# Kernel optimization log

Hardware: AMD Instinct MI355X
Metric: run time of the kernel (lower is better)

Reference implementation:

```python
import jax, jax.numpy as jnp
import numpy as np

N = 100000
E = 1600000
IN_C = 128
HID = 64
HEADS = 2
OUT_C = 64
Z = 16
NEG_SLOPE = 0.2


def _gat_layer(x, src, dst, W, a_src, a_dst, b, heads, d):
    # x: [N, in], W: [in, heads*d]
    h = (x @ W).reshape(-1, heads, d)                      # [N, H, d]
    alpha_s = (h * a_src).sum(-1)                          # [N, H]
    alpha_d = (h * a_dst).sum(-1)                          # [N, H]
    e = jax.nn.leaky_relu(alpha_s[src] + alpha_d[dst], NEG_SLOPE)  # [E, H]
    m = jax.ops.segment_max(e, dst, num_segments=N)        # [N, H]
    ex = jnp.exp(e - m[dst])
    denom = jax.ops.segment_sum(ex, dst, num_segments=N)   # [N, H]
    alpha = ex / (denom[dst] + 1e-16)                      # [E, H]
    out = jax.ops.segment_sum(h[src] * alpha[:, :, None], dst, num_segments=N)  # [N, H, d]
    return out.reshape(-1, heads * d) + b


def setup_inputs() -> dict:
    key = jax.random.key(0)
    ks = jax.random.split(key, 24)
    g = lambda k, shp, fan: jax.random.normal(k, shp, jnp.float32) * (1.0 / np.sqrt(fan))
    inp = {
        "x": jax.random.normal(ks[0], (N, IN_C), jnp.float32),
        "edge_index": jax.random.randint(ks[1], (2, E), 0, N, jnp.int64),
        "edge_attr": jax.random.normal(ks[2], (E, 8), jnp.float32),
        "eps": jax.random.normal(ks[3], (N, Z), jnp.float32),
        # GAT layer 1: heads=2, d=HID
        "W1": g(ks[4], (IN_C, HEADS * HID), IN_C),
        "a_src1": g(ks[5], (HEADS, HID), HID),
        "a_dst1": g(ks[6], (HEADS, HID), HID),
        "b1": jnp.zeros((HEADS * HID,), jnp.float32),
        # GAT layer 2: heads=1, d=OUT_C
        "W2": g(ks[7], (HEADS * HID, OUT_C), HEADS * HID),
        "a_src2": g(ks[8], (1, OUT_C), OUT_C),
        "a_dst2": g(ks[9], (1, OUT_C), OUT_C),
        "b2": jnp.zeros((OUT_C,), jnp.float32),
        # VAE
        "fc1_w": g(ks[10], (64, 128), 64), "fc1_b": jnp.zeros((128,), jnp.float32),
        "mu_w": g(ks[11], (128, Z), 128), "mu_b": jnp.zeros((Z,), jnp.float32),
        "lv_w": g(ks[12], (128, Z), 128), "lv_b": jnp.zeros((Z,), jnp.float32),
        "fc3_w": g(ks[13], (Z, 128), Z), "fc3_b": jnp.zeros((128,), jnp.float32),
        "fc4_w": g(ks[14], (128, 64), 128), "fc4_b": jnp.zeros((64,), jnp.float32),
    }
    return inp


def reference(x, edge_index, edge_attr, eps, W1, a_src1, a_dst1, b1, W2, a_src2, a_dst2, b2,
              fc1_w, fc1_b, mu_w, mu_b, lv_w, lv_b, fc3_w, fc3_b, fc4_w, fc4_b):
    src, dst = edge_index[0], edge_index[1]
    # GAT stack (edge_attr ignored: GATConv edge_dim=None)
    h = jax.nn.relu(_gat_layer(x, src, dst, W1, a_src1, a_dst1, b1, HEADS, HID))
    gat_out = _gat_layer(h, src, dst, W2, a_src2, a_dst2, b2, 1, OUT_C)  # [N, 64]
    # VAE
    h1 = jax.nn.relu(gat_out @ fc1_w + fc1_b)
    mu = h1 @ mu_w + mu_b
    logvar = h1 @ lv_w + lv_b
    lv = jnp.clip(logvar, -10.0, 10.0)
    z = mu + eps * jnp.exp(0.5 * lv)
    h3 = jax.nn.relu(z @ fc3_w + fc3_b)
    recon = h3 @ fc4_w + fc4_b
    return recon, mu, logvar, gat_out
```

## Files before the change

kernel.cpp:

```cpp
#include <hip/hip_runtime.h>
#include <hip/hip_bf16.h>

typedef __attribute__((ext_vector_type(8))) short bf16x8;
typedef __attribute__((ext_vector_type(4))) float f32x4;

__device__ __forceinline__ unsigned short f2b_bits(float x) {
    __hip_bfloat16 h = __float2bfloat16(x);
    unsigned short u;
    __builtin_memcpy(&u, &h, 2);
    return u;
}
__device__ __forceinline__ unsigned int pack2(float a, float b) {
    return (unsigned int)f2b_bits(a) | ((unsigned int)f2b_bits(b) << 16);
}
__device__ __forceinline__ float sx8(unsigned int w, int b) {
    return (float)((int)(w << (24 - 8 * b)) >> 24);
}

template<int FIN, int FOUT, int EPI, int HD, bool ABF, int ACT>
__global__ __launch_bounds__(256) void mfma_k(const void* __restrict__ Av,
                                              const float* __restrict__ W,
                                              const float* __restrict__ W2,
                                              const float* __restrict__ bias,
                                              const float* __restrict__ bias2,
                                              void* __restrict__ outv,
                                              void* __restrict__ out2,
                                              void* __restrict__ out3,
                                              float* __restrict__ scales,
                                              const float* __restrict__ asr,
                                              const float* __restrict__ adr,
                                              float* __restrict__ aso,
                                              float* __restrict__ ado,
                                              const float* __restrict__ epsp,
                                              int n)
{
    constexpr int KE = (FIN < 32) ? 32 : FIN;
    constexpr int KP = KE + 8;
    constexpr int KS = KE / 32;
    constexpr int NT = FOUT / 16;
    __shared__ __align__(16) unsigned short As[64 * KP];
    __shared__ __align__(16) unsigned short Wt[FOUT * KP];

    const int t  = threadIdx.x;
    const int m0 = blockIdx.x * 64;

    for (int idx = t; idx < 64 * (KE / 4); idx += 256) {
        int r  = idx / (KE / 4);
        int c4 = (idx % (KE / 4)) * 4;
        int row = m0 + r;
        unsigned int p0 = 0, p1 = 0;
        if (row < n && c4 < FIN) {
            if constexpr (ABF) {
                uint2 rv = *(const uint2*)((const unsigned short*)Av + (size_t)row * FIN + c4);
                p0 = rv.x; p1 = rv.y;
            } else {
                float4 v = *(const float4*)((const float*)Av + (size_t)row * FIN + c4);
                p0 = pack2(v.x, v.y); p1 = pack2(v.z, v.w);
            }
        }
        *(uint2*)(As + r * KP + c4) = make_uint2(p0, p1);
    }
    for (int idx = t; idx < KE * (FOUT / 4); idx += 256) {
        int k  = idx / (FOUT / 4);
        int c4 = (idx % (FOUT / 4)) * 4;
        float4 v = make_float4(0.f, 0.f, 0.f, 0.f);
        if (k < FIN) {
            if constexpr (EPI == 3) {
                v = (c4 < 16) ? *(const float4*)(W  + (size_t)k * 16 + c4)
                              : *(const float4*)(W2 + (size_t)k * 16 + (c4 - 16));
            } else {
                v = *(const float4*)(W + (size_t)k * FOUT + c4);
            }
        }
        Wt[(c4 + 0) * KP + k] = f2b_bits(v.x);
        Wt[(c4 + 1) * KP + k] = f2b_bits(v.y);
        Wt[(c4 + 2) * KP + k] = f2b_bits(v.z);
        Wt[(c4 + 3) * KP + k] = f2b_bits(v.w);
    }
    __syncthreads();

    const int w   = t >> 6;
    const int l   = t & 63;
    const int l15 = l & 15;
    const int g   = l >> 4;
    const int node = m0 + w * 16 + l15;

    f32x4 acc[NT];
    #pragma unroll
    for (int i = 0; i < NT; ++i) acc[i] = (f32x4){0.f, 0.f, 0.f, 0.f};

    #pragma unroll
    for (int ks = 0; ks < KS; ++ks) {
        bf16x8 nf = *(const bf16x8*)(As + (w * 16 + l15) * KP + ks * 32 + g * 8);
        #pragma unroll
        for (int tt = 0; tt < NT; ++tt) {
            bf16x8 wf = *(const bf16x8*)(Wt + (tt * 16 + l15) * KP + ks * 32 + g * 8);
            acc[tt] = __builtin_amdgcn_mfma_f32_16x16x32_bf16(wf, nf, acc[tt], 0, 0, 0);
        }
    }

    if constexpr (EPI == 0 || EPI == 1) {
        #pragma unroll
        for (int tt = 0; tt < NT; ++tt) {
            float4 bb = *(const float4*)(bias + 16 * tt + 4 * g);
            float o0 = acc[tt][0] + bb.x, o1 = acc[tt][1] + bb.y;
            float o2 = acc[tt][2] + bb.z, o3 = acc[tt][3] + bb.w;
            if (ACT == 1) {
                o0 = fmaxf(o0, 0.f); o1 = fmaxf(o1, 0.f);
                o2 = fmaxf(o2, 0.f); o3 = fmaxf(o3, 0.f);
            }
            if (node < n) {
                if constexpr (EPI == 0) {
                    *(float4*)((float*)outv + (size_t)node * FOUT + 16 * tt + 4 * g) =
                        make_float4(o0, o1, o2, o3);
                } else {
                    *(uint2*)((unsigned short*)outv + (size_t)node * FOUT + 16 * tt + 4 * g) =
                        make_uint2(pack2(o0, o1), pack2(o2, o3));
                }
            }
        }
    } else if constexpr (EPI == 2) {
        float amax = 0.f;
        float dsh[HD], ddh[HD];
        #pragma unroll
        for (int h = 0; h < HD; ++h) { dsh[h] = 0.f; ddh[h] = 0.f; }
        #pragma unroll
        for (int tt = 0; tt < NT; ++tt) {
            float4 av = *(const float4*)(asr + 16 * tt + 4 * g);
            float4 dv = *(const float4*)(adr + 16 * tt + 4 * g);
            const float* avp = (const float*)&av;
            const float* dvp = (const float*)&dv;
            constexpr int TPH = NT;
            const int h = (HD == 2) ? (tt / (NT / 2)) : 0;
            #pragma unroll
            for (int j = 0; j < 4; ++j) {
                float xv = acc[tt][j];
                amax = fmaxf(amax, fabsf(xv));
                dsh[h] = fmaf(xv, avp[j], dsh[h]);
                ddh[h] = fmaf(xv, dvp[j], ddh[h]);
            }
            (void)TPH;
        }
        amax = fmaxf(amax, __shfl_xor(amax, 16, 64));
        amax = fmaxf(amax, __shfl_xor(amax, 32, 64));
        #pragma unroll
        for (int h = 0; h < HD; ++h) {
            dsh[h] += __shfl_xor(dsh[h], 16, 64);
            dsh[h] += __shfl_xor(dsh[h], 32, 64);
            ddh[h] += __shfl_xor(ddh[h], 16, 64);
            ddh[h] += __shfl_xor(ddh[h], 32, 64);
        }
        float invsc = amax > 0.f ? 127.f / amax : 0.f;
        if (node < n) {
            #pragma unroll
            for (int tt = 0; tt < NT; ++tt) {
                int q0 = __float2int_rn(acc[tt][0] * invsc);
                int q1 = __float2int_rn(acc[tt][1] * invsc);
                int q2 = __float2int_rn(acc[tt][2] * invsc);
                int q3 = __float2int_rn(acc[tt][3] * invsc);
                unsigned int pv = (q0 & 255) | ((q1 & 255) << 8) |
                                  ((q2 & 255) << 16) | ((q3 & 255) << 24);
                ((unsigned int*)outv)[(size_t)node * (FOUT / 4) + 4 * tt + g] = pv;
            }
            if (g == 0) {
                scales[node] = amax * (1.f / 127.f);
                #pragma unroll
                for (int h = 0; h < HD; ++h) {
                    aso[(size_t)node * HD + h] = dsh[h];
                    ado[(size_t)node * HD + h] = ddh[h];
                }
            }
        }
    } else {
        float4 mb = *(const float4*)(bias  + 4 * g);
        float4 lb = *(const float4*)(bias2 + 4 * g);
        float mu0 = acc[0][0] + mb.x, mu1 = acc[0][1] + mb.y;
        float mu2 = acc[0][2] + mb.z, mu3 = acc[0][3] + mb.w;
        float lv0 = acc[1][0] + lb.x, lv1 = acc[1][1] + lb.y;
        float lv2 = acc[1][2] + lb.z, lv3 = acc[1][3] + lb.w;
        if (node < n) {
            float4 ep = *(const float4*)(epsp + (size_t)node * 16 + 4 * g);
            float z0 = fmaf(ep.x, __expf(0.5f * fminf(fmaxf(lv0, -10.f), 10.f)), mu0);
            float z1 = fmaf(ep.y, __expf(0.5f * fminf(fmaxf(lv1, -10.f), 10.f)), mu1);
            float z2 = fmaf(ep.z, __expf(0.5f * fminf(fmaxf(lv2, -10.f), 10.f)), mu2);
            float z3 = fmaf(ep.w, __expf(0.5f * fminf(fmaxf(lv3, -10.f), 10.f)), mu3);
            *(float4*)((float*)outv + (size_t)node * 16 + 4 * g) = make_float4(mu0, mu1, mu2, mu3);
            *(float4*)((float*)out2 + (size_t)node * 16 + 4 * g) = make_float4(lv0, lv1, lv2, lv3);
            *(uint2*)((unsigned short*)out3 + (size_t)node * 16 + 4 * g) =
                make_uint2(pack2(z0, z1), pack2(z2, z3));
        }
    }
}

__global__ __launch_bounds__(256) void count_k(const int* __restrict__ ei, int* __restrict__ deg, int E)
{
    int e = blockIdx.x * 256 + threadIdx.x;
    if (e >= E) return;
    atomicAdd(&deg[ei[E + e]], 1);
}

__global__ __launch_bounds__(256) void scanA_k(const int* __restrict__ deg, int* __restrict__ incl,
                                               int* __restrict__ bsum, int n)
{
    __shared__ int sh[256];
    int i = blockIdx.x * 256 + threadIdx.x;
    int v = (i < n) ? deg[i] : 0;
    sh[threadIdx.x] = v;
    __syncthreads();
    #pragma unroll
    for (int o = 1; o < 256; o <<= 1) {
        int t = (threadIdx.x >= o) ? sh[threadIdx.x - o] : 0;
        __syncthreads();
        sh[threadIdx.x] += t;
        __syncthreads();
    }
    if (i < n) incl[i] = sh[threadIdx.x];
    if (threadIdx.x == 255) bsum[blockIdx.x] = sh[255];
}

__global__ __launch_bounds__(512) void scanB_k(int* __restrict__ bsum, int nb)
{
    __shared__ int sh[512];
    int v = (threadIdx.x < nb) ? bsum[threadIdx.x] : 0;
    sh[threadIdx.x] = v;
    __syncthreads();
    #pragma unroll
    for (int o = 1; o < 512; o <<= 1) {
        int t = (threadIdx.x >= o) ? sh[threadIdx.x - o] : 0;
        __syncthreads();
        sh[threadIdx.x] += t;
        __syncthreads();
    }
    if (threadIdx.x < nb) bsum[threadIdx.x] = sh[threadIdx.x] - v;
}

__global__ __launch_bounds__(256) void scanC_k(const int* __restrict__ deg, const int* __restrict__ incl,
                                               const int* __restrict__ bsum, int* __restrict__ off,
                                               int* __restrict__ cursor, int n, int E)
{
    int i = blockIdx.x * 256 + threadIdx.x;
    if (i >= n) return;
    int v = incl[i] - deg[i] + bsum[i >> 8];
    off[i] = v;
    cursor[i] = v;
    if (i == 0) off[n] = E;
}

__global__ __launch_bounds__(256) void scatter_k(const int* __restrict__ ei, int* __restrict__ cursor,
                                                 int* __restrict__ csr_src, int E, int n)
{
    const int grp = blockIdx.x & 7;
    const int bin = blockIdx.x >> 3;
    const int bpg = gridDim.x >> 3;
    const int rsz = (n + 7) >> 3;
    const int lo = grp * rsz;
    const int hi = min(n, lo + rsz);
    const int stride = bpg * 256;
    for (int e = bin * 256 + threadIdx.x; e < E; e += stride) {
        int d = ei[E + e];
        if (d >= lo && d < hi) {
            int pos = atomicAdd(&cursor[d], 1);
            csr_src[pos] = ei[e];
        }
    }
}

template<int FEAT, int H, int ACT, bool OUTB>
__global__ __launch_bounds__(256) void gat_agg_k(const int* __restrict__ csr_src,
                                                 const int* __restrict__ off,
                                                 const float* __restrict__ as_,
                                                 const float* __restrict__ ad_,
                                                 const unsigned int* __restrict__ h8,
                                                 const float* __restrict__ sc,
                                                 const float* __restrict__ bias,
                                                 void* __restrict__ outv, int n)
{
    constexpr int LANES = 16;
    constexpr int FPL   = FEAT / LANES;
    constexpr int WPR   = FEAT / 4;
    constexpr int SUBL  = LANES / H;
    constexpr int NCH   = 4;
    const int tid = blockIdx.x * 256 + threadIdx.x;
    const int d = tid >> 4;
    if (d >= n) return;
    const int lane = threadIdx.x & 15;
    const int myhead = lane / SUBL;
    const int sl = lane % SUBL;
    const int start = off[d], end = off[d + 1];
    const float adm = ad_[d * H + myhead];

    float vreg[NCH], sreg_sc[NCH]; int sreg[NCH];
    float m = -3.4e38f;
    #pragma unroll
    for (int c = 0; c < NCH; ++c) {
        int j = start + sl + c * SUBL;
        int s = 0; float v = -3.4e38f, scl = 0.f;
        if (j < end) {
            s = csr_src[j];
            v = as_[s * H + myhead] + adm;
            v = v > 0.f ? v : 0.2f * v;
            scl = sc[s];
        }
        sreg[c] = s; vreg[c] = v; sreg_sc[c] = scl;
        m = fmaxf(m, v);
    }
    for (int j = start + sl + NCH * SUBL; j < end; j += SUBL) {
        int s = csr_src[j];
        float v = as_[s * H + myhead] + adm;
        v = v > 0.f ? v : 0.2f * v;
        m = fmaxf(m, v);
    }
    #pragma unroll
    for (int o = SUBL / 2; o > 0; o >>= 1)
        m = fmaxf(m, __shfl_xor(m, o, SUBL));

    float ssum = 0.f;
    #pragma unroll
    for (int c = 0; c < NCH; ++c)
        if (start + sl + c * SUBL < end) ssum += __expf(vreg[c] - m);
    for (int j = start + sl + NCH * SUBL; j < end; j += SUBL) {
        int s = csr_src[j];
        float v = as_[s * H + myhead] + adm;
        v = v > 0.f ? v : 0.2f * v;
        ssum += __expf(v - m);
    }
    #pragma unroll
    for (int o = SUBL / 2; o > 0; o >>= 1)
        ssum += __shfl_xor(ssum, o, SUBL);
    const float inv = 1.f / (ssum + 1e-16f);

    float acc[FPL];
    #pragma unroll
    for (int k = 0; k < FPL; ++k) acc[k] = 0.f;

    auto body = [&](float a, int s) {
        if constexpr (FPL == 8) {
            uint2 r = ((const uint2*)(h8 + (size_t)s * WPR))[lane];
            acc[0] = fmaf(sx8(r.x, 0), a, acc[0]);
            acc[1] = fmaf(sx8(r.x, 1), a, acc[1]);
            acc[2] = fmaf(sx8(r.x, 2), a, acc[2]);
            acc[3] = fmaf(sx8(r.x, 3), a, acc[3]);
            acc[4] = fmaf(sx8(r.y, 0), a, acc[4]);
            acc[5] = fmaf(sx8(r.y, 1), a, acc[5]);
            acc[6] = fmaf(sx8(r.y, 2), a, acc[6]);
            acc[7] = fmaf(sx8(r.y, 3), a, acc[7]);
        } else {
            unsigned int r = (h8 + (size_t)s * WPR)[lane];
            acc[0] = fmaf(sx8(r, 0), a, acc[0]);
            acc[1] = fmaf(sx8(r, 1), a, acc[1]);
            acc[2] = fmaf(sx8(r, 2), a, acc[2]);
            acc[3] = fmaf(sx8(r, 3), a, acc[3]);
        }
    };

    const int nch = (end - start + SUBL - 1) / SUBL;
    for (int c = 0; c < nch; ++c) {
        const int j0 = start + c * SUBL;
        const int cnt = min(SUBL, end - j0);
        float myalpha = 0.f; int mysrc = 0;
        if (c < NCH) {
            mysrc = sreg[c];
            if (sl < cnt) myalpha = __expf(vreg[c] - m) * inv * sreg_sc[c];
        } else {
            if (sl < cnt) {
                mysrc = csr_src[j0 + sl];
                float v = as_[mysrc * H + myhead] + adm;
                v = v > 0.f ? v : 0.2f * v;
                myalpha = __expf(v - m) * inv * sc[mysrc];
            }
        }
        if (cnt == SUBL) {
            #pragma unroll
            for (int u = 0; u < SUBL; ++u) {
                float a = __shfl(myalpha, myhead * SUBL + u, LANES);
                int   s = __shfl(mysrc, u, LANES);
                body(a, s);
            }
        } else {
            for (int u = 0; u < cnt; ++u) {
                float a = __shfl(myalpha, myhead * SUBL + u, LANES);
                int   s = __shfl(mysrc, u, LANES);
                body(a, s);
            }
        }
    }

    if constexpr (OUTB) {
        float o[FPL];
        #pragma unroll
        for (int k = 0; k < FPL; ++k) {
            o[k] = acc[k] + bias[lane * FPL + k];
            if (ACT == 1) o[k] = fmaxf(o[k], 0.f);
        }
        uint4 pv;
        pv.x = pack2(o[0], o[1]); pv.y = pack2(o[2], o[3]);
        pv.z = pack2(o[4], o[5]); pv.w = pack2(o[6], o[7]);
        *(uint4*)((unsigned short*)outv + (size_t)d * FEAT + lane * FPL) = pv;
    } else {
        float* outf = (float*)outv;
        #pragma unroll
        for (int k = 0; k < FPL; ++k) {
            float o = acc[k] + bias[lane * FPL + k];
            if (ACT == 1) o = fmaxf(o, 0.f);
            outf[(size_t)d * FEAT + lane * FPL + k] = o;
        }
    }
}

extern "C" void kernel_launch(void* const* d_in, const int* in_sizes, int n_in,
                              void* d_out, int out_size, void* d_ws, size_t ws_size,
                              hipStream_t stream)
{
    const int n = in_sizes[0] / 128;
    const int E = in_sizes[1] / 2;

    const float* x   = (const float*)d_in[0];
    const int*   ei  = (const int*)d_in[1];
    const float* eps = (const float*)d_in[3];
    const float* W1  = (const float*)d_in[4];
    const float* as1w= (const float*)d_in[5];
    const float* ad1w= (const float*)d_in[6];
    const float* b1  = (const float*)d_in[7];
    const float* W2  = (const float*)d_in[8];
    const float* as2w= (const float*)d_in[9];
    const float* ad2w= (const float*)d_in[10];
    const float* b2  = (const float*)d_in[11];
    const float* fc1w= (const float*)d_in[12];
    const float* fc1b= (const float*)d_in[13];
    const float* muw = (const float*)d_in[14];
    const float* mub = (const float*)d_in[15];
    const float* lvw = (const float*)d_in[16];
    const float* lvb = (const float*)d_in[17];
    const float* fc3w= (const float*)d_in[18];
    const float* fc3b= (const float*)d_in[19];
    const float* fc4w= (const float*)d_in[20];
    const float* fc4b= (const float*)d_in[21];

    char* ws = (char*)d_ws;

    size_t oDeg   = 0;
    size_t oOff   = oDeg  + (size_t)n * 4;
    size_t oIncl  = oOff  + (size_t)(n + 1) * 4;
    size_t oCur   = oIncl + (size_t)n * 4;
    size_t oBsum  = oCur  + (size_t)n * 4;
    size_t oCsr   = oBsum + 512 * 4;
    size_t oR1    = oCsr  + (size_t)E * 4;
    size_t oR2    = oR1   + (size_t)n * 256;
    size_t oR3    = oR2   + (size_t)n * 256;
    size_t oAS1   = oR3   + (size_t)n * 128;
    size_t oAD1   = oAS1  + (size_t)n * 2 * 4;
    size_t oAS2   = oAD1  + (size_t)n * 2 * 4;
    size_t oAD2   = oAS2  + (size_t)n * 4;
    size_t oSC1   = oAD2  + (size_t)n * 4;
    size_t oSC2   = oSC1  + (size_t)n * 4;

    int* deg    = (int*)(ws + oDeg);
    int* off    = (int*)(ws + oOff);
    int* incl   = (int*)(ws + oIncl);
    int* cursor = (int*)(ws + oCur);
    int* bsum   = (int*)(ws + oBsum);
    int* csr    = (int*)(ws + oCsr);
    unsigned int*   h1q  = (unsigned int*)(ws + oR1);
    unsigned short* h1v  = (unsigned short*)(ws + oR1);
    unsigned short* hl2b = (unsigned short*)(ws + oR2);
    unsigned short* h3   = (unsigned short*)(ws + oR2);
    unsigned int*   h2q  = (unsigned int*)(ws + oR3);
    unsigned short* zb   = (unsigned short*)(ws + oR3);
    float* as1  = (float*)(ws + oAS1);
    float* ad1  = (float*)(ws + oAD1);
    float* as2  = (float*)(ws + oAS2);
    float* ad2  = (float*)(ws + oAD2);
    float* sc1  = (float*)(ws + oSC1);
    float* sc2  = (float*)(ws + oSC2);

    float* out     = (float*)d_out;
    float* o_recon = out;
    float* o_mu    = out + (size_t)n * 64;
    float* o_lv    = out + (size_t)n * 80;
    float* o_gat   = out + (size_t)n * 96;

    const int ebl  = (E + 255) / 256;
    const int nbS  = (n + 255) / 256;
    const int abl  = (n * 16 + 255) / 256;
    const int g64  = (n + 63) / 64;

    hipMemsetAsync(deg, 0, (size_t)n * 4, stream);
    count_k<<<ebl, 256, 0, stream>>>(ei, deg, E);
    scanA_k<<<nbS, 256, 0, stream>>>(deg, incl, bsum, n);
    scanB_k<<<1, 512, 0, stream>>>(bsum, nbS);
    scanC_k<<<nbS, 256, 0, stream>>>(deg, incl, bsum, off, cursor, n, E);
    scatter_k<<<1024, 256, 0, stream>>>(ei, cursor, csr, E, n);

    mfma_k<128, 128, 2, 2, false, 0><<<g64, 256, 0, stream>>>(
        x, W1, nullptr, nullptr, nullptr, h1q, nullptr, nullptr,
        sc1, as1w, ad1w, as1, ad1, nullptr, n);
    gat_agg_k<128, 2, 1, true><<<abl, 256, 0, stream>>>(
        csr, off, as1, ad1, h1q, sc1, b1, hl2b, n);

    mfma_k<128, 64, 2, 1, true, 0><<<g64, 256, 0, stream>>>(
        hl2b, W2, nullptr, nullptr, nullptr, h2q, nullptr, nullptr,
        sc2, as2w, ad2w, as2, ad2, nullptr, n);
    gat_agg_k<64, 1, 0, false><<<abl, 256, 0, stream>>>(
        csr, off, as2, ad2, h2q, sc2, b2, o_gat, n);

    mfma_k<64, 128, 1, 0, false, 1><<<g64, 256, 0, stream>>>(
        o_gat, fc1w, nullptr, fc1b, nullptr, h1v, nullptr, nullptr,
        nullptr, nullptr, nullptr, nullptr, nullptr, nullptr, n);
    mfma_k<128, 32, 3, 0, true, 0><<<g64, 256, 0, stream>>>(
        h1v, muw, lvw, mub, lvb, o_mu, o_lv, zb,
        nullptr, nullptr, nullptr, nullptr, nullptr, eps, n);
    mfma_k<16, 128, 1, 0, true, 1><<<g64, 256, 0, stream>>>(
        zb, fc3w, nullptr, fc3b, nullptr, h3, nullptr, nullptr,
        nullptr, nullptr, nullptr, nullptr, nullptr, nullptr, n);
    mfma_k<128, 64, 0, 0, true, 0><<<g64, 256, 0, stream>>>(
        h3, fc4w, nullptr, fc4b, nullptr, o_recon, nullptr, nullptr,
        nullptr, nullptr, nullptr, nullptr, nullptr, nullptr, n);
}
```

Baseline: 423.6 us.

## Bucket CSR edges by source range within each destination for gather locality

```diff
diff --git a/kernel.cpp b/kernel.cpp
--- a/kernel.cpp
+++ b/kernel.cpp
@@ -130,7 +130,6 @@
             float4 dv = *(const float4*)(adr + 16 * tt + 4 * g);
             const float* avp = (const float*)&av;
             const float* dvp = (const float*)&dv;
-            constexpr int TPH = NT;
             const int h = (HD == 2) ? (tt / (NT / 2)) : 0;
             #pragma unroll
             for (int j = 0; j < 4; ++j) {
@@ -139,7 +138,6 @@
                 dsh[h] = fmaf(xv, avp[j], dsh[h]);
                 ddh[h] = fmaf(xv, dvp[j], ddh[h]);
             }
-            (void)TPH;
         }
         amax = fmaxf(amax, __shfl_xor(amax, 16, 64));
         amax = fmaxf(amax, __shfl_xor(amax, 32, 64));
@@ -192,19 +190,21 @@
     }
 }
 
-__global__ __launch_bounds__(256) void count_k(const int* __restrict__ ei, int* __restrict__ deg, int E)
+__global__ __launch_bounds__(256) void count_k(const int* __restrict__ ei, int* __restrict__ cnt,
+                                               int E, int bshift)
 {
     int e = blockIdx.x * 256 + threadIdx.x;
     if (e >= E) return;
-    atomicAdd(&deg[ei[E + e]], 1);
-}
-
-__global__ __launch_bounds__(256) void scanA_k(const int* __restrict__ deg, int* __restrict__ incl,
-                                               int* __restrict__ bsum, int n)
+    int s = ei[e], d = ei[E + e];
+    atomicAdd(&cnt[d * 8 + (s >> bshift)], 1);
+}
+
+__global__ __launch_bounds__(256) void scanA_k(const int* __restrict__ cnt, int* __restrict__ incl,
+                                               int* __restrict__ bsum, int m)
 {
     __shared__ int sh[256];
     int i = blockIdx.x * 256 + threadIdx.x;
-    int v = (i < n) ? deg[i] : 0;
+    int v = (i < m) ? cnt[i] : 0;
     sh[threadIdx.x] = v;
     __syncthreads();
     #pragma unroll
@@ -214,40 +214,50 @@
         sh[threadIdx.x] += t;
         __syncthreads();
     }
-    if (i < n) incl[i] = sh[threadIdx.x];
+    if (i < m) incl[i] = sh[threadIdx.x];
     if (threadIdx.x == 255) bsum[blockIdx.x] = sh[255];
 }
 
 __global__ __launch_bounds__(512) void scanB_k(int* __restrict__ bsum, int nb)
 {
     __shared__ int sh[512];
-    int v = (threadIdx.x < nb) ? bsum[threadIdx.x] : 0;
-    sh[threadIdx.x] = v;
+    __shared__ int carrysh;
+    if (threadIdx.x == 0) carrysh = 0;
     __syncthreads();
-    #pragma unroll
-    for (int o = 1; o < 512; o <<= 1) {
-        int t = (threadIdx.x >= o) ? sh[threadIdx.x - o] : 0;
+    for (int base = 0; base < nb; base += 512) {
+        int i = base + threadIdx.x;
+        int v = (i < nb) ? bsum[i] : 0;
+        sh[threadIdx.x] = v;
         __syncthreads();
-        sh[threadIdx.x] += t;
+        #pragma unroll
+        for (int o = 1; o < 512; o <<= 1) {
+            int t = (threadIdx.x >= o) ? sh[threadIdx.x - o] : 0;
+            __syncthreads();
+            sh[threadIdx.x] += t;
+            __syncthreads();
+        }
+        int c = carrysh;
+        if (i < nb) bsum[i] = c + sh[threadIdx.x] - v;
         __syncthreads();
-    }
-    if (threadIdx.x < nb) bsum[threadIdx.x] = sh[threadIdx.x] - v;
-}
-
-__global__ __launch_bounds__(256) void scanC_k(const int* __restrict__ deg, const int* __restrict__ incl,
+        if (threadIdx.x == 511) carrysh = c + sh[511];
+        __syncthreads();
+    }
+}
+
+__global__ __launch_bounds__(256) void scanC_k(const int* __restrict__ cnt, const int* __restrict__ incl,
                                                const int* __restrict__ bsum, int* __restrict__ off,
-                                               int* __restrict__ cursor, int n, int E)
+                                               int* __restrict__ cursor, int m, int E)
 {
     int i = blockIdx.x * 256 + threadIdx.x;
-    if (i >= n) return;
-    int v = incl[i] - deg[i] + bsum[i >> 8];
+    if (i >= m) return;
+    int v = incl[i] - cnt[i] + bsum[i >> 8];
     off[i] = v;
     cursor[i] = v;
-    if (i == 0) off[n] = E;
+    if (i == 0) off[m] = E;
 }
 
 __global__ __launch_bounds__(256) void scatter_k(const int* __restrict__ ei, int* __restrict__ cursor,
-                                                 int* __restrict__ csr_src, int E, int n)
+                                                 int* __restrict__ csr_src, int E, int n, int bshift)
 {
     const int grp = blockIdx.x & 7;
     const int bin = blockIdx.x >> 3;
@@ -259,8 +269,9 @@
     for (int e = bin * 256 + threadIdx.x; e < E; e += stride) {
         int d = ei[E + e];
         if (d >= lo && d < hi) {
-            int pos = atomicAdd(&cursor[d], 1);
-            csr_src[pos] = ei[e];
+            int s = ei[e];
+            int pos = atomicAdd(&cursor[d * 8 + (s >> bshift)], 1);
+            csr_src[pos] = s;
         }
     }
 }
@@ -286,7 +297,7 @@
     const int lane = threadIdx.x & 15;
     const int myhead = lane / SUBL;
     const int sl = lane % SUBL;
-    const int start = off[d], end = off[d + 1];
+    const int start = off[d * 8], end = off[d * 8 + 8];
     const float adm = ad_[d * H + myhead];
 
     float vreg[NCH], sreg_sc[NCH]; int sreg[NCH];
@@ -413,6 +424,10 @@
 {
     const int n = in_sizes[0] / 128;
     const int E = in_sizes[1] / 2;
+    const int m8 = n * 8;
+
+    int bshift = 0;
+    while (((n - 1) >> bshift) >= 8) ++bshift;
 
     const float* x   = (const float*)d_in[0];
     const int*   ei  = (const int*)d_in[1];
@@ -438,12 +453,12 @@
 
     char* ws = (char*)d_ws;
 
-    size_t oDeg   = 0;
-    size_t oOff   = oDeg  + (size_t)n * 4;
-    size_t oIncl  = oOff  + (size_t)(n + 1) * 4;
-    size_t oCur   = oIncl + (size_t)n * 4;
-    size_t oBsum  = oCur  + (size_t)n * 4;
-    size_t oCsr   = oBsum + 512 * 4;
+    size_t oCnt   = 0;
+    size_t oOff   = oCnt  + (size_t)m8 * 4;
+    size_t oIncl  = oOff  + (size_t)(m8 + 1) * 4;
+    size_t oCur   = oIncl + (size_t)m8 * 4;
+    size_t oBsum  = oCur  + (size_t)m8 * 4;
+    size_t oCsr   = oBsum + 4096 * 4;
     size_t oR1    = oCsr  + (size_t)E * 4;
     size_t oR2    = oR1   + (size_t)n * 256;
     size_t oR3    = oR2   + (size_t)n * 256;
@@ -453,8 +468,9 @@
     size_t oAD2   = oAS2  + (size_t)n * 4;
     size_t oSC1   = oAD2  + (size_t)n * 4;
     size_t oSC2   = oSC1  + (size_t)n * 4;
-
-    int* deg    = (int*)(ws + oDeg);
+    (void)oSC2;
+
+    int* cnt    = (int*)(ws + oCnt);
     int* off    = (int*)(ws + oOff);
     int* incl   = (int*)(ws + oIncl);
     int* cursor = (int*)(ws + oCur);
@@ -480,16 +496,16 @@
     float* o_gat   = out + (size_t)n * 96;
 
     const int ebl  = (E + 255) / 256;
-    const int nbS  = (n + 255) / 256;
+    const int nbS8 = (m8 + 255) / 256;
     const int abl  = (n * 16 + 255) / 256;
     const int g64  = (n + 63) / 64;
 
-    hipMemsetAsync(deg, 0, (size_t)n * 4, stream);
-    count_k<<<ebl, 256, 0, stream>>>(ei, deg, E);
-    scanA_k<<<nbS, 256, 0, stream>>>(deg, incl, bsum, n);
-    scanB_k<<<1, 512, 0, stream>>>(bsum, nbS);
-    scanC_k<<<nbS, 256, 0, stream>>>(deg, incl, bsum, off, cursor, n, E);
-    scatter_k<<<1024, 256, 0, stream>>>(ei, cursor, csr, E, n);
+    hipMemsetAsync(cnt, 0, (size_t)m8 * 4, stream);
+    count_k<<<ebl, 256, 0, stream>>>(ei, cnt, E, bshift);
+    scanA_k<<<nbS8, 256, 0, stream>>>(cnt, incl, bsum, m8);
+    scanB_k<<<1, 512, 0, stream>>>(bsum, nbS8);
+    scanC_k<<<nbS8, 256, 0, stream>>>(cnt, incl, bsum, off, cursor, m8, E);
+    scatter_k<<<1024, 256, 0, stream>>>(ei, cursor, csr, E, n, bshift);
 
     mfma_k<128, 128, 2, 2, false, 0><<<g64, 256, 0, stream>>>(
         x, W1, nullptr, nullptr, nullptr, h1q, nullptr, nullptr,
```

After: 424.4 us. Within noise of the previous version (+0.2%).
